# Kernel tuning notes

Hardware: AMD Instinct MI355X
Metric: run time of the kernel (lower is better)

Reference implementation:

```python
import jax, jax.numpy as jnp
import numpy as np

N_NODES = 100000
N_EDGES = 1600000
IN_DIM = 64
HEADS = [4, 4]
DIMS = [16, 16]


def gat_layer(x, src, dst, W, al, ar, b, n_nodes):
    """DGL-style GATConv: x [N,F] -> [N,H,D]."""
    H, D = al.shape
    z = (x @ W).reshape(-1, H, D)                      # [N,H,D]
    el = jnp.sum(z * al, axis=-1)                      # [N,H]
    er = jnp.sum(z * ar, axis=-1)                      # [N,H]
    e = jax.nn.leaky_relu(el[src] + er[dst], 0.2)      # [E,H] edge scores
    # numerically-stable edge softmax over incoming edges of each dst node
    m = jax.ops.segment_max(e, dst, num_segments=n_nodes)
    m = jnp.where(jnp.isfinite(m), m, 0.0)
    ex = jnp.exp(e - jax.lax.stop_gradient(m)[dst])    # [E,H]
    denom = jax.ops.segment_sum(ex, dst, num_segments=n_nodes)
    alpha = ex / jnp.maximum(denom[dst], 1e-9)         # [E,H]
    # scatter-aggregate messages alpha * z[src]
    out = jax.ops.segment_sum(alpha[:, :, None] * z[src], dst, num_segments=n_nodes)
    return out + b.reshape(H, D)


def setup_inputs() -> dict:
    key = jax.random.key(0)
    ks = jax.random.split(key, 16)
    feat = jax.random.normal(ks[0], (N_NODES, IN_DIM), dtype=jnp.float32)
    src = jax.random.randint(ks[1], (N_EDGES,), 0, N_NODES, dtype=jnp.int32)
    dst = jax.random.randint(ks[2], (N_EDGES,), 0, N_NODES, dtype=jnp.int32)
    def lin(k, fi, fo):
        return jax.random.normal(k, (fi, fo), dtype=jnp.float32) * (1.0 / np.sqrt(fi))
    H0, D0 = HEADS[0], DIMS[0]
    H1, D1 = HEADS[1], DIMS[1]
    inp = {
        "feat": feat, "src": src, "dst": dst,
        "W0": lin(ks[3], IN_DIM, H0 * D0),
        "al0": jax.random.normal(ks[4], (H0, D0), jnp.float32) * 0.1,
        "ar0": jax.random.normal(ks[5], (H0, D0), jnp.float32) * 0.1,
        "b0": jnp.zeros((H0 * D0,), jnp.float32),
        "W1": lin(ks[6], H0 * D0, H1 * D1),
        "al1": jax.random.normal(ks[7], (H1, D1), jnp.float32) * 0.1,
        "ar1": jax.random.normal(ks[8], (H1, D1), jnp.float32) * 0.1,
        "b1": jnp.zeros((H1 * D1,), jnp.float32),
        "Wo": lin(ks[9], H1 * D1, 1),
        "alo": jax.random.normal(ks[10], (1, 1), jnp.float32) * 0.1,
        "aro": jax.random.normal(ks[11], (1, 1), jnp.float32) * 0.1,
        "bo": jnp.zeros((1,), jnp.float32),
    }
    return inp


def reference(feat, src, dst, W0, al0, ar0, b0, W1, al1, ar1, b1, Wo, alo, aro, bo):
    n = feat.shape[0]
    h = gat_layer(feat, src, dst, W0, al0, ar0, b0, n)       # [N,H0,D0]
    h = jax.nn.relu(h).reshape(n, -1)                         # head concat
    h = gat_layer(h, src, dst, W1, al1, ar1, b1, n)           # [N,H1,D1]
    h = jax.nn.relu(h).reshape(n, -1)
    out = gat_layer(h, src, dst, Wo, alo, aro, bo, n)         # [N,1,1]
    return jnp.squeeze(out, axis=1)                           # [N,1]
```

## Files before the change

kernel.cpp:

```cpp
#include <hip/hip_runtime.h>
#include <hip/hip_fp16.h>
#include <math.h>

#define NN 100000
#define NE 1600000
#define NBUK 391
#define CAP 4608
#define EPB 4096

__device__ __forceinline__ float leaky02(float v) {
    return v > 0.0f ? v : 0.2f * v;
}


__global__ __launch_bounds__(256) void k_bucket(
    const int* __restrict__ src, const int* __restrict__ dst,
    int* __restrict__ bucketCnt, int* __restrict__ gBuf)
{
    __shared__ int stg[EPB];
    __shared__ int tgt[EPB];
    __shared__ int lcnt[NBUK];
    __shared__ int lexc[NBUK];
    __shared__ int lgb[NBUK];
    __shared__ int totalLocal;
    const int t = threadIdx.x;
    const int e0 = blockIdx.x * EPB;

    for (int i = t; i < NBUK; i += 256) lcnt[i] = 0;
    __syncthreads();

    int bk[16], pk[16];
    #pragma unroll
    for (int j = 0; j < 16; ++j) {
        const int e = e0 + j * 256 + t;
        if (e < NE) {
            const int d = dst[e];
            bk[j] = d >> 8;
            pk[j] = (src[e] << 8) | (d & 255);
            atomicAdd(&lcnt[bk[j]], 1);
        } else bk[j] = -1;
    }
    __syncthreads();

    if (t < 64) {
        int carry = 0;
        for (int c = 0; c < NBUK; c += 64) {
            const int idx = c + t;
            int v = (idx < NBUK) ? lcnt[idx] : 0;
            int inc = v;
            #pragma unroll
            for (int off = 1; off < 64; off <<= 1) {
                int u = __shfl_up(inc, off, 64);
                if (t >= off) inc += u;
            }
            if (idx < NBUK) lexc[idx] = carry + inc - v;
            carry += __shfl(inc, 63, 64);
        }
        if (t == 0) totalLocal = carry;
    }
    __syncthreads();

    for (int i = t; i < NBUK; i += 256) {
        const int c = lcnt[i];
        lgb[i] = c ? atomicAdd(&bucketCnt[i], c) : 0;
        lcnt[i] = 0;
    }
    __syncthreads();

    #pragma unroll
    for (int j = 0; j < 16; ++j) {
        if (bk[j] >= 0) {
            const int r = atomicAdd(&lcnt[bk[j]], 1);
            const int p = lexc[bk[j]] + r;
            stg[p] = pk[j];
            int slot = lgb[bk[j]] + r;
            if (slot >= CAP) slot = CAP - 1;
            tgt[p] = bk[j] * CAP + slot;
        }
    }
    __syncthreads();

    const int tot = totalLocal;
    for (int i = t; i < tot; i += 256)
        gBuf[tgt[i]] = stg[i];
}

__global__ __launch_bounds__(64) void k_bbase(
    const int* __restrict__ bucketCnt, int* __restrict__ bucketBase,
    int* __restrict__ row_ptr)
{
    const int t = threadIdx.x;
    int carry = 0;
    for (int c = 0; c < NBUK; c += 64) {
        const int idx = c + t;
        int v = (idx < NBUK) ? bucketCnt[idx] : 0;
        int inc = v;
        #pragma unroll
        for (int off = 1; off < 64; off <<= 1) {
            int u = __shfl_up(inc, off, 64);
            if (t >= off) inc += u;
        }
        if (idx < NBUK) bucketBase[idx] = carry + inc - v;
        carry += __shfl(inc, 63, 64);
    }
    if (t == 0) row_ptr[NN] = NE;
}

__global__ __launch_bounds__(256) void k_csr_local(
    const int* __restrict__ bucketCnt, const int* __restrict__ bucketBase,
    const int* __restrict__ gBuf,
    int* __restrict__ row_ptr, int* __restrict__ ssrc)
{
    __shared__ int stg2[CAP];
    __shared__ int stg3[CAP];
    __shared__ int c2[256];
    __shared__ int sc[256];
    const int t = threadIdx.x;
    const int k = blockIdx.x;
    const int cnt = min(bucketCnt[k], CAP);
    const int gb  = bucketBase[k];

    c2[t] = 0;
    __syncthreads();
    for (int i = t; i < cnt; i += 256) {
        const int pk = gBuf[k * CAP + i];
        stg2[i] = pk;
        atomicAdd(&c2[pk & 255], 1);
    }
    __syncthreads();
    if (t < 64) {
        int carry = 0;
        for (int c = 0; c < 256; c += 64) {
            int v = c2[c + t];
            int inc = v;
            #pragma unroll
            for (int off = 1; off < 64; off <<= 1) {
                int u = __shfl_up(inc, off, 64);
                if (t >= off) inc += u;
            }
            sc[c + t] = carry + inc - v;
            carry += __shfl(inc, 63, 64);
        }
    }
    __syncthreads();
    const int node = (k << 8) + t;
    if (node < NN) row_ptr[node] = gb + sc[t];
    c2[t] = 0;
    __syncthreads();
    for (int i = t; i < cnt; i += 256) {
        const int pk = stg2[i];
        const int dl = pk & 255;
        const int r = atomicAdd(&c2[dl], 1);
        stg3[sc[dl] + r] = pk >> 8;
    }
    __syncthreads();
    for (int i = t; i < cnt; i += 256)
        ssrc[gb + i] = stg3[i];
}


__global__ __launch_bounds__(256) void k_node_prep(
    const float* __restrict__ xin, const float* __restrict__ W,
    const float* __restrict__ al, const float* __restrict__ ar,
    __half* __restrict__ z, float* __restrict__ el, float* __restrict__ er)
{
    const int t = threadIdx.x;
    const int lane = t & 63;
    const int wvU = __builtin_amdgcn_readfirstlane(t >> 6);
    const int nodeBase = blockIdx.x * 64 + wvU * 16;

    float wc[64];
    #pragma unroll
    for (int k = 0; k < 64; ++k) wc[k] = W[k * 64 + lane];
    const float a_l = al[lane], a_r = ar[lane];

    #pragma unroll 1
    for (int i = 0; i < 16; i += 2) {
        const int nA = nodeBase + i;
        if (nA >= NN) break;
        const int nB = nA + 1;
        const bool hasB = (nB < NN);
        const float4* __restrict__ xA4 = (const float4*)(xin + (size_t)nA * 64);
        const float4* __restrict__ xB4 = (const float4*)(xin + (size_t)(hasB ? nB : nA) * 64);

        float accA = 0.f, accB = 0.f;
        #pragma unroll
        for (int k4 = 0; k4 < 16; ++k4) {
            const float4 a4 = xA4[k4];
            const float4 b4 = xB4[k4];
            const float w0 = wc[k4 * 4 + 0], w1 = wc[k4 * 4 + 1];
            const float w2 = wc[k4 * 4 + 2], w3 = wc[k4 * 4 + 3];
            accA += a4.x * w0 + a4.y * w1 + a4.z * w2 + a4.w * w3;
            accB += b4.x * w0 + b4.y * w1 + b4.z * w2 + b4.w * w3;
        }

        {
            z[(size_t)nA * 64 + lane] = __float2half(accA);
            float pl = accA * a_l, pr = accA * a_r;
            #pragma unroll
            for (int off = 8; off > 0; off >>= 1) {
                pl += __shfl_xor(pl, off, 16);
                pr += __shfl_xor(pr, off, 16);
            }
            if ((lane & 15) == 0) {
                const int h = lane >> 4;
                el[nA * 4 + h] = pl;
                er[nA * 4 + h] = pr;
            }
        }
        if (hasB) {
            z[(size_t)nB * 64 + lane] = __float2half(accB);
            float pl = accB * a_l, pr = accB * a_r;
            #pragma unroll
            for (int off = 8; off > 0; off >>= 1) {
                pl += __shfl_xor(pl, off, 16);
                pr += __shfl_xor(pr, off, 16);
            }
            if ((lane & 15) == 0) {
                const int h = lane >> 4;
                el[nB * 4 + h] = pl;
                er[nB * 4 + h] = pr;
            }
        }
    }
}

__global__ __launch_bounds__(256) void k_csr_agg(
    const int* __restrict__ row_ptr, const int* __restrict__ ssrc,
    const float* __restrict__ el, const float* __restrict__ er,
    const __half* __restrict__ z, const float* __restrict__ b,
    float* __restrict__ xout,
    const float* __restrict__ Wo,
    float* __restrict__ zo)
{
    const int t = threadIdx.x;
    const int wv = t >> 6, l = t & 63;
    const int sg = l >> 4, sl = l & 15;
    const int eh = l & 3;
    const int hh = sl >> 2;
    const int n = blockIdx.x * 4 + wv;
    const int beg = row_ptr[n], deg = row_ptr[n + 1] - beg;
    const float er_eh = er[n * 4 + eh];

    float4 acc = {0.f, 0.f, 0.f, 0.f};
    float den4 = 0.f;
    for (int base = 0; base < deg; base += 16) {
        const int myE = base + (l >> 2);
        int s = 0; float x = 0.f;
        if (myE < deg) {
            s = ssrc[beg + myE];
            x = __expf(leaky02(el[s * 4 + eh] + er_eh));
        }
        den4 += x;
        const int rem = deg - base;
        const int nk = (min(rem, 16) + 3) >> 2;
        for (int k = 0; k < nk; ++k) {
            const int ec = k * 4 + sg;
            const int   sj = __shfl(s, ec * 4, 64);
            const float xj = __shfl(x, ec * 4 + hh, 64);
            const uint2 raw = *(const uint2*)(z + (size_t)sj * 64 + sl * 4);
            const float2 f01 = __half22float2(*(const __half2*)&raw.x);
            const float2 f23 = __half22float2(*(const __half2*)&raw.y);
            acc.x += xj * f01.x; acc.y += xj * f01.y;
            acc.z += xj * f23.x; acc.w += xj * f23.y;
        }
    }
    #pragma unroll
    for (int off = 16; off < 64; off <<= 1) {
        acc.x += __shfl_xor(acc.x, off, 64);
        acc.y += __shfl_xor(acc.y, off, 64);
        acc.z += __shfl_xor(acc.z, off, 64);
        acc.w += __shfl_xor(acc.w, off, 64);
    }
    #pragma unroll
    for (int off = 4; off < 64; off <<= 1) den4 += __shfl_xor(den4, off, 64);
    const float den = fmaxf(__shfl(den4, hh, 64), 1e-9f);

    const float4 b4 = *(const float4*)(b + sl * 4);
    float4 v;
    v.x = fmaxf(acc.x / den + b4.x, 0.f);
    v.y = fmaxf(acc.y / den + b4.y, 0.f);
    v.z = fmaxf(acc.z / den + b4.z, 0.f);
    v.w = fmaxf(acc.w / den + b4.w, 0.f);

    if (xout) {
        if (l < 16) *(float4*)(xout + (size_t)n * 64 + sl * 4) = v;
    } else {
        const float4 w4 = *(const float4*)(Wo + sl * 4);
        float p = v.x * w4.x + v.y * w4.y + v.z * w4.z + v.w * w4.w;
        #pragma unroll
        for (int off = 1; off < 16; off <<= 1) p += __shfl_xor(p, off, 64);
        if (l == 0) zo[n] = p;
    }
}


__global__ __launch_bounds__(256) void k_csr_agg_o(
    const int* __restrict__ row_ptr, const int* __restrict__ ssrc,
    const float* __restrict__ zo, const float* __restrict__ alo,
    const float* __restrict__ aro, const float* __restrict__ bo,
    float* __restrict__ out)
{
    const int t = threadIdx.x, l = t & 15;
    const int n = blockIdx.x * 16 + (t >> 4);
    const float a = alo[0];
    const float zr = aro[0] * zo[n];
    const int beg = row_ptr[n], end = row_ptr[n + 1];

    float den = 0.f, accv = 0.f;
    for (int i = beg + l; i < end; i += 16) {
        const float zs = zo[ssrc[i]];
        const float ex = __expf(leaky02(a * zs + zr));
        den += ex; accv += ex * zs;
    }
    #pragma unroll
    for (int off = 8; off; off >>= 1) {
        den  += __shfl_xor(den, off, 16);
        accv += __shfl_xor(accv, off, 16);
    }
    if (l == 0) out[n] = accv / fmaxf(den, 1e-9f) + bo[0];
}


extern "C" void kernel_launch(void* const* d_in, const int* in_sizes, int n_in,
                              void* d_out, int out_size, void* d_ws, size_t ws_size,
                              hipStream_t stream) {
    const float* feat = (const float*)d_in[0];
    const int*   src  = (const int*)d_in[1];
    const int*   dst  = (const int*)d_in[2];
    const float* W0   = (const float*)d_in[3];
    const float* al0  = (const float*)d_in[4];
    const float* ar0  = (const float*)d_in[5];
    const float* b0   = (const float*)d_in[6];
    const float* W1   = (const float*)d_in[7];
    const float* al1  = (const float*)d_in[8];
    const float* ar1  = (const float*)d_in[9];
    const float* b1   = (const float*)d_in[10];
    const float* Wo   = (const float*)d_in[11];
    const float* alo  = (const float*)d_in[12];
    const float* aro  = (const float*)d_in[13];
    const float* bo   = (const float*)d_in[14];
    float* out = (float*)d_out;

    int* bucketCnt  = (int*)d_ws;
    int* bucketBase = bucketCnt + NBUK;
    int* row_ptr    = bucketBase + NBUK;
    int* gBuf       = row_ptr + (NN + 2);
    int* ssrc       = gBuf + (size_t)NBUK * CAP;
    __half* z  = (__half*)(ssrc + NE);
    float* xA  = (float*)(z + (size_t)NN * 64);
    float* el  = xA + (size_t)NN * 64;
    float* er  = el + (size_t)NN * 4;
    float* zo  = er + (size_t)NN * 4;

    const int gPrep = (NN + 63) / 64;
    const int gN16  = NN / 16;
    const int gAgg  = NN / 4;

    hipMemsetAsync(bucketCnt, 0, NBUK * sizeof(int), stream);
    k_bucket   <<<NBUK, 256, 0, stream>>>(src, dst, bucketCnt, gBuf);
    k_bbase    <<<1, 64, 0, stream>>>(bucketCnt, bucketBase, row_ptr);
    k_csr_local<<<NBUK, 256, 0, stream>>>(bucketCnt, bucketBase, gBuf,
                                          row_ptr, ssrc);

    k_node_prep<<<gPrep, 256, 0, stream>>>(feat, W0, al0, ar0, z, el, er);
    k_csr_agg  <<<gAgg, 256, 0, stream>>>(row_ptr, ssrc, el, er, z, b0,
                                          xA, nullptr, nullptr);

    k_node_prep<<<gPrep, 256, 0, stream>>>(xA, W1, al1, ar1, z, el, er);
    k_csr_agg  <<<gAgg, 256, 0, stream>>>(row_ptr, ssrc, el, er, z, b1,
                                          nullptr, Wo, zo);

    k_csr_agg_o<<<gN16, 256, 0, stream>>>(row_ptr, ssrc, zo, alo, aro, bo, out);
}
```

Baseline: 285.4 us.

## Fold bucket-base scan into CSR kernel, halve edges per bucket block, simplify aggregation loop

The bucketing kernel now handles half as many edges per block, so roughly twice as many blocks launch. The separate single-block scan kernel is removed: each CSR-local block computes its own global base by summing the counts of the preceding buckets with a shared-memory reduction. The aggregation kernel drops the shuffle-based edge broadcast. Each 16-lane group walks the edges directly, computing exp scores per head and processing two edges per iteration, and the final division becomes a multiply by a reciprocal. The trade-off is redundant prefix summing in every CSR block and some duplicated el/exp work across lanes of the same head.

```diff
diff --git a/kernel.cpp b/kernel.cpp
--- a/kernel.cpp
+++ b/kernel.cpp
@@ -6,7 +6,7 @@
 #define NE 1600000
 #define NBUK 391
 #define CAP 4608
-#define EPB 4096
+#define EPB 2048
 
 __device__ __forceinline__ float leaky02(float v) {
     return v > 0.0f ? v : 0.2f * v;
@@ -29,9 +29,9 @@
     for (int i = t; i < NBUK; i += 256) lcnt[i] = 0;
     __syncthreads();
 
-    int bk[16], pk[16];
-    #pragma unroll
-    for (int j = 0; j < 16; ++j) {
+    int bk[8], pk[8];
+    #pragma unroll
+    for (int j = 0; j < 8; ++j) {
         const int e = e0 + j * 256 + t;
         if (e < NE) {
             const int d = dst[e];
@@ -68,7 +68,7 @@
     __syncthreads();
 
     #pragma unroll
-    for (int j = 0; j < 16; ++j) {
+    for (int j = 0; j < 8; ++j) {
         if (bk[j] >= 0) {
             const int r = atomicAdd(&lcnt[bk[j]], 1);
             const int p = lexc[bk[j]] + r;
@@ -85,40 +85,28 @@
         gBuf[tgt[i]] = stg[i];
 }
 
-__global__ __launch_bounds__(64) void k_bbase(
-    const int* __restrict__ bucketCnt, int* __restrict__ bucketBase,
-    int* __restrict__ row_ptr)
-{
-    const int t = threadIdx.x;
-    int carry = 0;
-    for (int c = 0; c < NBUK; c += 64) {
-        const int idx = c + t;
-        int v = (idx < NBUK) ? bucketCnt[idx] : 0;
-        int inc = v;
-        #pragma unroll
-        for (int off = 1; off < 64; off <<= 1) {
-            int u = __shfl_up(inc, off, 64);
-            if (t >= off) inc += u;
-        }
-        if (idx < NBUK) bucketBase[idx] = carry + inc - v;
-        carry += __shfl(inc, 63, 64);
-    }
-    if (t == 0) row_ptr[NN] = NE;
-}
-
 __global__ __launch_bounds__(256) void k_csr_local(
-    const int* __restrict__ bucketCnt, const int* __restrict__ bucketBase,
-    const int* __restrict__ gBuf,
+    const int* __restrict__ bucketCnt, const int* __restrict__ gBuf,
     int* __restrict__ row_ptr, int* __restrict__ ssrc)
 {
     __shared__ int stg2[CAP];
     __shared__ int stg3[CAP];
     __shared__ int c2[256];
     __shared__ int sc[256];
+    __shared__ int red[256];
     const int t = threadIdx.x;
     const int k = blockIdx.x;
     const int cnt = min(bucketCnt[k], CAP);
-    const int gb  = bucketBase[k];
+
+    int part = 0;
+    for (int j = t; j < k; j += 256) part += bucketCnt[j];
+    red[t] = part;
+    __syncthreads();
+    for (int s2 = 128; s2; s2 >>= 1) {
+        if (t < s2) red[t] += red[t + s2];
+        __syncthreads();
+    }
+    const int gb = red[0];
 
     c2[t] = 0;
     __syncthreads();
@@ -145,6 +133,7 @@
     __syncthreads();
     const int node = (k << 8) + t;
     if (node < NN) row_ptr[node] = gb + sc[t];
+    if (k == NBUK - 1 && t == 0) row_ptr[NN] = NE;
     c2[t] = 0;
     __syncthreads();
     for (int i = t; i < cnt; i += 256) {
@@ -236,52 +225,57 @@
     const int t = threadIdx.x;
     const int wv = t >> 6, l = t & 63;
     const int sg = l >> 4, sl = l & 15;
-    const int eh = l & 3;
     const int hh = sl >> 2;
     const int n = blockIdx.x * 4 + wv;
-    const int beg = row_ptr[n], deg = row_ptr[n + 1] - beg;
-    const float er_eh = er[n * 4 + eh];
+    const int beg = row_ptr[n], end = row_ptr[n + 1];
+    const float er_hh = er[n * 4 + hh];
 
     float4 acc = {0.f, 0.f, 0.f, 0.f};
-    float den4 = 0.f;
-    for (int base = 0; base < deg; base += 16) {
-        const int myE = base + (l >> 2);
-        int s = 0; float x = 0.f;
-        if (myE < deg) {
-            s = ssrc[beg + myE];
-            x = __expf(leaky02(el[s * 4 + eh] + er_eh));
-        }
-        den4 += x;
-        const int rem = deg - base;
-        const int nk = (min(rem, 16) + 3) >> 2;
-        for (int k = 0; k < nk; ++k) {
-            const int ec = k * 4 + sg;
-            const int   sj = __shfl(s, ec * 4, 64);
-            const float xj = __shfl(x, ec * 4 + hh, 64);
-            const uint2 raw = *(const uint2*)(z + (size_t)sj * 64 + sl * 4);
-            const float2 f01 = __half22float2(*(const __half2*)&raw.x);
-            const float2 f23 = __half22float2(*(const __half2*)&raw.y);
-            acc.x += xj * f01.x; acc.y += xj * f01.y;
-            acc.z += xj * f23.x; acc.w += xj * f23.y;
-        }
-    }
+    float den = 0.f;
+    int i = beg + sg;
+    for (; i + 4 < end; i += 8) {
+        const int s0 = ssrc[i], s1 = ssrc[i + 4];
+        const float x0 = __expf(leaky02(el[s0 * 4 + hh] + er_hh));
+        const float x1 = __expf(leaky02(el[s1 * 4 + hh] + er_hh));
+        const uint2 r0 = *(const uint2*)(z + (size_t)s0 * 64 + sl * 4);
+        const uint2 r1 = *(const uint2*)(z + (size_t)s1 * 64 + sl * 4);
+        den += x0 + x1;
+        const float2 p0 = __half22float2(*(const __half2*)&r0.x);
+        const float2 q0 = __half22float2(*(const __half2*)&r0.y);
+        const float2 p1 = __half22float2(*(const __half2*)&r1.x);
+        const float2 q1 = __half22float2(*(const __half2*)&r1.y);
+        acc.x += x0 * p0.x + x1 * p1.x;
+        acc.y += x0 * p0.y + x1 * p1.y;
+        acc.z += x0 * q0.x + x1 * q1.x;
+        acc.w += x0 * q0.y + x1 * q1.y;
+    }
+    if (i < end) {
+        const int s0 = ssrc[i];
+        const float x0 = __expf(leaky02(el[s0 * 4 + hh] + er_hh));
+        const uint2 r0 = *(const uint2*)(z + (size_t)s0 * 64 + sl * 4);
+        den += x0;
+        const float2 p0 = __half22float2(*(const __half2*)&r0.x);
+        const float2 q0 = __half22float2(*(const __half2*)&r0.y);
+        acc.x += x0 * p0.x; acc.y += x0 * p0.y;
+        acc.z += x0 * q0.x; acc.w += x0 * q0.y;
+    }
+
     #pragma unroll
     for (int off = 16; off < 64; off <<= 1) {
         acc.x += __shfl_xor(acc.x, off, 64);
         acc.y += __shfl_xor(acc.y, off, 64);
         acc.z += __shfl_xor(acc.z, off, 64);
         acc.w += __shfl_xor(acc.w, off, 64);
-    }
-    #pragma unroll
-    for (int off = 4; off < 64; off <<= 1) den4 += __shfl_xor(den4, off, 64);
-    const float den = fmaxf(__shfl(den4, hh, 64), 1e-9f);
+        den   += __shfl_xor(den,   off, 64);
+    }
+    const float dinv = 1.0f / fmaxf(den, 1e-9f);
 
     const float4 b4 = *(const float4*)(b + sl * 4);
     float4 v;
-    v.x = fmaxf(acc.x / den + b4.x, 0.f);
-    v.y = fmaxf(acc.y / den + b4.y, 0.f);
-    v.z = fmaxf(acc.z / den + b4.z, 0.f);
-    v.w = fmaxf(acc.w / den + b4.w, 0.f);
+    v.x = fmaxf(acc.x * dinv + b4.x, 0.f);
+    v.y = fmaxf(acc.y * dinv + b4.y, 0.f);
+    v.z = fmaxf(acc.z * dinv + b4.z, 0.f);
+    v.w = fmaxf(acc.w * dinv + b4.w, 0.f);
 
     if (xout) {
         if (l < 16) *(float4*)(xout + (size_t)n * 64 + sl * 4) = v;
@@ -343,8 +337,7 @@
     float* out = (float*)d_out;
 
     int* bucketCnt  = (int*)d_ws;
-    int* bucketBase = bucketCnt + NBUK;
-    int* row_ptr    = bucketBase + NBUK;
+    int* row_ptr    = bucketCnt + NBUK;
     int* gBuf       = row_ptr + (NN + 2);
     int* ssrc       = gBuf + (size_t)NBUK * CAP;
     __half* z  = (__half*)(ssrc + NE);
@@ -353,15 +346,14 @@
     float* er  = el + (size_t)NN * 4;
     float* zo  = er + (size_t)NN * 4;
 
+    const int gBkt  = (NE + EPB - 1) / EPB;
     const int gPrep = (NN + 63) / 64;
     const int gN16  = NN / 16;
     const int gAgg  = NN / 4;
 
     hipMemsetAsync(bucketCnt, 0, NBUK * sizeof(int), stream);
-    k_bucket   <<<NBUK, 256, 0, stream>>>(src, dst, bucketCnt, gBuf);
-    k_bbase    <<<1, 64, 0, stream>>>(bucketCnt, bucketBase, row_ptr);
-    k_csr_local<<<NBUK, 256, 0, stream>>>(bucketCnt, bucketBase, gBuf,
-                                          row_ptr, ssrc);
+    k_bucket   <<<gBkt, 256, 0, stream>>>(src, dst, bucketCnt, gBuf);
+    k_csr_local<<<NBUK, 256, 0, stream>>>(bucketCnt, gBuf, row_ptr, ssrc);
 
     k_node_prep<<<gPrep, 256, 0, stream>>>(feat, W0, al0, ar0, z, el, er);
     k_csr_agg  <<<gAgg, 256, 0, stream>>>(row_ptr, ssrc, el, er, z, b0,
```

Result: no change. 280.5 us (-1.7%).
